# Kernel optimization log

Hardware: AMD Instinct MI355X
Metric: run time of the kernel (lower is better)

Reference implementation:

```python
import jax, jax.numpy as jnp
import numpy as np

B, L, H, NF = 8192, 2048, 2048, 8  # batch, latent, h_last_dim, n_flows


def setup_inputs() -> dict:
    key = jax.random.key(0)
    k0, k1, k2, k3 = jax.random.split(key, 4)
    scale = 0.02  # keep v well-conditioned through repeated linears
    return {
        "z": jax.random.normal(k0, (B, L), jnp.float32),
        "h_last": jax.random.normal(k1, (B, H), jnp.float32),
        "W0": jax.random.normal(k2, (L, H), jnp.float32) * scale,
        "b0": jnp.zeros((L,), jnp.float32),
        "Ws": jax.random.normal(k3, (NF - 1, L, L), jnp.float32) * scale,
        "bs": jnp.zeros((NF - 1, L), jnp.float32),
    }


def _hflow(v, z):
    # z_new = z - 2 * v (v . z) / ||v||^2  (Householder reflection, O(L) form of
    # the original's explicit vv^T bmm)
    vz = jnp.sum(v * z, axis=1, keepdims=True)       # [B,1]
    norm_sq = jnp.sum(v * v, axis=1, keepdims=True)  # [B,1]
    return z - 2.0 * v * (vz / norm_sq)


def reference(z, h_last, W0, b0, Ws, bs):
    # first v from h_last, then chain: v_{j+1} = Linear(v_j), z_{j+1} = HF(v_{j+1}, z_j)
    v = h_last @ W0.T + b0
    z = _hflow(v, z)

    def step(carry, wb):
        v, z = carry
        W, b = wb
        v = v @ W.T + b
        z = _hflow(v, z)
        return (v, z), None

    (v, z), _ = jax.lax.scan(step, (v, z), (Ws, bs))
    return z
```

## Files before the change

kernel.cpp:

```cpp
#include <hip/hip_runtime.h>
#include <hip/hip_bf16.h>
#include <stdint.h>

#define B_  8192
#define L_  2048
#define NF_ 8

typedef __bf16 bf16_t;
typedef __bf16 bf16x8 __attribute__((ext_vector_type(8)));
typedef __bf16 bf16x4 __attribute__((ext_vector_type(4)));
typedef float  floatx4 __attribute__((ext_vector_type(4)));

__device__ __forceinline__ bf16_t f2bf(float f) {
    union { float f; uint32_t u; } a; a.f = f;
    uint32_t r = a.u + 0x7fffu + ((a.u >> 16) & 1u);
    union { uint16_t s; bf16_t b; } o; o.s = (uint16_t)(r >> 16);
    return o.b;
}

#define GLD16(gp, lp)                                                          \
    __builtin_amdgcn_global_load_lds(                                          \
        (const __attribute__((address_space(1))) void*)(gp),                   \
        (__attribute__((address_space(3))) void*)(lp), 16, 0, 0)

__global__ __launch_bounds__(256) void cvt_kernel(const float* __restrict__ s,
                                                  bf16_t* __restrict__ d) {
    const int i = blockIdx.x * 256 + threadIdx.x;
    float4 f = ((const float4*)s)[i];
    bf16x4 o = { f2bf(f.x), f2bf(f.y), f2bf(f.z), f2bf(f.w) };
    ((bf16x4*)d)[i] = o;
}

__global__ __launch_bounds__(256, 4) void gemm_bt_kernel(
    const bf16_t* __restrict__ A,
    const bf16_t* __restrict__ W,
    const float*  __restrict__ bias,
    bf16_t* __restrict__ Vb)
{
    constexpr int K = L_;
    constexpr int N = L_;
    __shared__ alignas(16) bf16_t sA[128 * 64];
    __shared__ alignas(16) bf16_t sB[128 * 64];

    const int tid  = threadIdx.x;
    const int lane = tid & 63;
    const int wave = tid >> 6;
    const int wm   = wave >> 1;
    const int wn   = wave & 1;
    const int tm   = blockIdx.y * 128;
    const int tn   = blockIdx.x * 128;

    const int srow = tid >> 3;
    const int schk = (tid & 7) ^ (srow & 7);
    const bf16_t* Ag = A + (size_t)(tm + srow) * K + schk * 8;
    const bf16_t* Wg = W + (size_t)(tn + srow) * K + schk * 8;
    bf16_t* sAp = sA + tid * 8;
    bf16_t* sBp = sB + tid * 8;

    floatx4 acc[4][4] = {};

    const int ra = wm * 64 + (lane & 15);
    const int rb = wn * 64 + (lane & 15);
    const int q  = lane >> 4;
    const int rx = lane & 7;

    for (int kt = 0; kt < K; kt += 64) {
#pragma unroll
        for (int i = 0; i < 4; ++i) {
            GLD16(Ag + kt + (size_t)(32 * i) * K, sAp + i * 2048);
            GLD16(Wg + kt + (size_t)(32 * i) * K, sBp + i * 2048);
        }
        asm volatile("s_waitcnt vmcnt(0)" ::: "memory");
        __syncthreads();

#pragma unroll
        for (int ks = 0; ks < 2; ++ks) {
            const int c = ks * 4 + q;
            const int pc = (c ^ rx) * 8;
            bf16x8 af[4], bw[4];
#pragma unroll
            for (int i = 0; i < 4; ++i) {
                af[i] = *(const bf16x8*)(sA + (ra + i * 16) * 64 + pc);
                bw[i] = *(const bf16x8*)(sB + (rb + i * 16) * 64 + pc);
            }
#pragma unroll
            for (int mi = 0; mi < 4; ++mi)
#pragma unroll
                for (int ni = 0; ni < 4; ++ni)
                    acc[mi][ni] = __builtin_amdgcn_mfma_f32_16x16x32_bf16(
                        af[mi], bw[ni], acc[mi][ni], 0, 0, 0);
        }
        __syncthreads();
    }

    const int row0 = tm + wm * 64 + (lane >> 4) * 4;
    const int col0 = tn + wn * 64 + (lane & 15);
#pragma unroll
    for (int ni = 0; ni < 4; ++ni) {
        const int col = col0 + ni * 16;
        const float bv = bias[col];
#pragma unroll
        for (int mi = 0; mi < 4; ++mi) {
#pragma unroll
            for (int r = 0; r < 4; ++r) {
                Vb[(size_t)(row0 + mi * 16 + r) * N + col] = f2bf(acc[mi][ni][r] + bv);
            }
        }
    }
}

__global__ __launch_bounds__(256) void hflowN_kernel(
    const bf16_t* __restrict__ Vall,
    int nf,
    const float* __restrict__ zin, float* __restrict__ zout)
{
    const int lane = threadIdx.x & 63;
    const int row  = blockIdx.x * 4 + (threadIdx.x >> 6);
    const float4* z4 = (const float4*)(zin + (size_t)row * L_);
    float4*       zo = (float4*)(zout + (size_t)row * L_);

    float4 z[8];
#pragma unroll
    for (int j = 0; j < 4; ++j) {
        const int idx = lane + 64 * j;
        z[2 * j]     = z4[2 * idx];
        z[2 * j + 1] = z4[2 * idx + 1];
    }

    const size_t vstride = (size_t)B_ * L_;
    const bf16x8* v8 = (const bf16x8*)(Vall + (size_t)row * L_);

    bf16x8 vcur[4];
#pragma unroll
    for (int j = 0; j < 4; ++j) vcur[j] = v8[lane + 64 * j];

    for (int f = 0; f < nf; ++f) {
        bf16x8 vnxt[4];
        if (f + 1 < nf) {
            const bf16x8* vn = (const bf16x8*)((const bf16_t*)v8 + (size_t)(f + 1) * vstride);
#pragma unroll
            for (int j = 0; j < 4; ++j) vnxt[j] = vn[lane + 64 * j];
        }

        float vf[32];
#pragma unroll
        for (int j = 0; j < 4; ++j)
#pragma unroll
            for (int e = 0; e < 8; ++e) vf[j * 8 + e] = (float)vcur[j][e];

        float vz = 0.f, vv = 0.f;
#pragma unroll
        for (int j = 0; j < 4; ++j) {
            const float* fp = vf + j * 8;
            vz += fp[0] * z[2*j].x + fp[1] * z[2*j].y + fp[2] * z[2*j].z + fp[3] * z[2*j].w
                + fp[4] * z[2*j+1].x + fp[5] * z[2*j+1].y + fp[6] * z[2*j+1].z + fp[7] * z[2*j+1].w;
            vv += fp[0]*fp[0] + fp[1]*fp[1] + fp[2]*fp[2] + fp[3]*fp[3]
                + fp[4]*fp[4] + fp[5]*fp[5] + fp[6]*fp[6] + fp[7]*fp[7];
        }

#pragma unroll
        for (int off = 1; off < 64; off <<= 1) {
            vz += __shfl_xor(vz, off);
            vv += __shfl_xor(vv, off);
        }
        const float s = 2.0f * vz / vv;

#pragma unroll
        for (int j = 0; j < 4; ++j) {
            const float* fp = vf + j * 8;
            z[2*j].x -= s * fp[0]; z[2*j].y -= s * fp[1];
            z[2*j].z -= s * fp[2]; z[2*j].w -= s * fp[3];
            z[2*j+1].x -= s * fp[4]; z[2*j+1].y -= s * fp[5];
            z[2*j+1].z -= s * fp[6]; z[2*j+1].w -= s * fp[7];
        }

#pragma unroll
        for (int j = 0; j < 4; ++j) vcur[j] = vnxt[j];
    }

#pragma unroll
    for (int j = 0; j < 4; ++j) {
        const int idx = lane + 64 * j;
        zo[2 * idx]     = z[2 * j];
        zo[2 * idx + 1] = z[2 * j + 1];
    }
}

extern "C" void kernel_launch(void* const* d_in, const int* in_sizes, int n_in,
                              void* d_out, int out_size, void* d_ws, size_t ws_size,
                              hipStream_t stream) {
    (void)in_sizes; (void)n_in; (void)out_size;
    const float* z_in   = (const float*)d_in[0];
    const float* h_last = (const float*)d_in[1];
    const float* W0     = (const float*)d_in[2];
    const float* b0     = (const float*)d_in[3];
    const float* Wsp    = (const float*)d_in[4];
    const float* bsp    = (const float*)d_in[5];
    float* z_out = (float*)d_out;

    char* ws = (char*)d_ws;
    const size_t wbytes = (size_t)NF_ * L_ * L_ * 2;
    const size_t vbytes = (size_t)B_ * L_ * 2;

    bf16_t* Wbf = (bf16_t*)ws;
    cvt_kernel<<<(L_ * L_) / 1024, 256, 0, stream>>>(W0, Wbf);
    cvt_kernel<<<((NF_ - 1) * L_ * L_) / 1024, 256, 0, stream>>>(
        Wsp, Wbf + (size_t)L_ * L_);

    dim3 ggrid(L_ / 128, B_ / 128);

    if (ws_size >= wbytes + vbytes + (size_t)NF_ * vbytes) {
        bf16_t* Hbf  = (bf16_t*)(ws + wbytes);
        bf16_t* Vall = Hbf + (size_t)B_ * L_;
        cvt_kernel<<<(B_ * L_) / 1024, 256, 0, stream>>>(h_last, Hbf);

        for (int j = 0; j < NF_; ++j) {
            const float* bias = (j == 0) ? b0 : bsp + (size_t)(j - 1) * L_;
            const bf16_t* Wj = Wbf + (size_t)j * L_ * L_;
            const bf16_t* Ain = (j == 0) ? Hbf : Vall + (size_t)(j - 1) * B_ * L_;
            bf16_t* Vout = Vall + (size_t)j * B_ * L_;
            gemm_bt_kernel<<<ggrid, 256, 0, stream>>>(Ain, Wj, bias, Vout);
        }
        hflowN_kernel<<<B_ / 4, 256, 0, stream>>>(Vall, NF_, z_in, z_out);
    } else {
        bf16_t* Vp0 = (bf16_t*)(ws + wbytes);
        bf16_t* Vp1 = Vp0 + (size_t)B_ * L_;
        cvt_kernel<<<(B_ * L_) / 1024, 256, 0, stream>>>(h_last, Vp0);

        bf16_t* bufs[2] = { Vp0, Vp1 };
        for (int j = 0; j < NF_; ++j) {
            const float* bias = (j == 0) ? b0 : bsp + (size_t)(j - 1) * L_;
            const bf16_t* Wj = Wbf + (size_t)j * L_ * L_;
            bf16_t* Ain = bufs[j & 1];
            bf16_t* Vout = bufs[(j + 1) & 1];
            gemm_bt_kernel<<<ggrid, 256, 0, stream>>>(Ain, Wj, bias, Vout);
            hflowN_kernel<<<B_ / 4, 256, 0, stream>>>(
                Vout, 1, (j == 0) ? z_in : z_out, z_out);
        }
    }
}
```

Before: 889.1 us.

## Rewrite GEMM with 256x256 tiles, 4-stage LDS pipeline, and fused conversion kernel

```diff
diff --git a/kernel.cpp b/kernel.cpp
--- a/kernel.cpp
+++ b/kernel.cpp
@@ -23,87 +23,140 @@
         (const __attribute__((address_space(1))) void*)(gp),                   \
         (__attribute__((address_space(3))) void*)(lp), 16, 0, 0)
 
-__global__ __launch_bounds__(256) void cvt_kernel(const float* __restrict__ s,
-                                                  bf16_t* __restrict__ d) {
-    const int i = blockIdx.x * 256 + threadIdx.x;
-    float4 f = ((const float4*)s)[i];
-    bf16x4 o = { f2bf(f.x), f2bf(f.y), f2bf(f.z), f2bf(f.w) };
-    ((bf16x4*)d)[i] = o;
-}
-
-__global__ __launch_bounds__(256, 4) void gemm_bt_kernel(
+__global__ __launch_bounds__(256) void cvt3_kernel(
+    const float* __restrict__ sa, bf16_t* __restrict__ da, int na,
+    const float* __restrict__ sb, bf16_t* __restrict__ db, int nb,
+    const float* __restrict__ sc, bf16_t* __restrict__ dc, int nc)
+{
+    const int total = na + nb + nc;
+    for (int i = blockIdx.x * 256 + threadIdx.x; i < total;
+         i += gridDim.x * 256) {
+        const float* s; bf16_t* d; int j = i;
+        if (j < na)            { s = sa; d = da; }
+        else { j -= na;
+            if (j < nb)        { s = sb; d = db; }
+            else { j -= nb;      s = sc; d = dc; } }
+        float4 f = ((const float4*)s)[j];
+        bf16x4 o = { f2bf(f.x), f2bf(f.y), f2bf(f.z), f2bf(f.w) };
+        ((bf16x4*)d)[j] = o;
+    }
+}
+
+#define VM4  asm volatile("s_waitcnt vmcnt(4)" ::: "memory")
+#define VM0  asm volatile("s_waitcnt vmcnt(0)" ::: "memory")
+#define VMX  do {} while (0)
+
+__global__ __launch_bounds__(512, 2) void gemm_bt_kernel(
     const bf16_t* __restrict__ A,
     const bf16_t* __restrict__ W,
     const float*  __restrict__ bias,
     bf16_t* __restrict__ Vb)
 {
-    constexpr int K = L_;
-    constexpr int N = L_;
-    __shared__ alignas(16) bf16_t sA[128 * 64];
-    __shared__ alignas(16) bf16_t sB[128 * 64];
+    constexpr int K  = L_;
+    constexpr int N  = L_;
+    constexpr int NT = K / 32;
+    __shared__ alignas(16) bf16_t lds[4][16384];
 
     const int tid  = threadIdx.x;
     const int lane = tid & 63;
     const int wave = tid >> 6;
-    const int wm   = wave >> 1;
-    const int wn   = wave & 1;
-    const int tm   = blockIdx.y * 128;
-    const int tn   = blockIdx.x * 128;
-
-    const int srow = tid >> 3;
-    const int schk = (tid & 7) ^ (srow & 7);
-    const bf16_t* Ag = A + (size_t)(tm + srow) * K + schk * 8;
-    const bf16_t* Wg = W + (size_t)(tn + srow) * K + schk * 8;
-    bf16_t* sAp = sA + tid * 8;
-    bf16_t* sBp = sB + tid * 8;
-
-    floatx4 acc[4][4] = {};
-
-    const int ra = wm * 64 + (lane & 15);
-    const int rb = wn * 64 + (lane & 15);
-    const int q  = lane >> 4;
-    const int rx = lane & 7;
-
-    for (int kt = 0; kt < K; kt += 64) {
-#pragma unroll
-        for (int i = 0; i < 4; ++i) {
-            GLD16(Ag + kt + (size_t)(32 * i) * K, sAp + i * 2048);
-            GLD16(Wg + kt + (size_t)(32 * i) * K, sBp + i * 2048);
-        }
-        asm volatile("s_waitcnt vmcnt(0)" ::: "memory");
-        __syncthreads();
-
-#pragma unroll
-        for (int ks = 0; ks < 2; ++ks) {
-            const int c = ks * 4 + q;
-            const int pc = (c ^ rx) * 8;
-            bf16x8 af[4], bw[4];
-#pragma unroll
-            for (int i = 0; i < 4; ++i) {
-                af[i] = *(const bf16x8*)(sA + (ra + i * 16) * 64 + pc);
-                bw[i] = *(const bf16x8*)(sB + (rb + i * 16) * 64 + pc);
-            }
-#pragma unroll
-            for (int mi = 0; mi < 4; ++mi)
-#pragma unroll
-                for (int ni = 0; ni < 4; ++ni)
-                    acc[mi][ni] = __builtin_amdgcn_mfma_f32_16x16x32_bf16(
-                        af[mi], bw[ni], acc[mi][ni], 0, 0, 0);
-        }
-        __syncthreads();
-    }
-
-    const int row0 = tm + wm * 64 + (lane >> 4) * 4;
-    const int col0 = tn + wn * 64 + (lane & 15);
-#pragma unroll
-    for (int ni = 0; ni < 4; ++ni) {
-        const int col = col0 + ni * 16;
-        const float bv = bias[col];
-#pragma unroll
-        for (int mi = 0; mi < 4; ++mi) {
-#pragma unroll
-            for (int r = 0; r < 4; ++r) {
-                Vb[(size_t)(row0 + mi * 16 + r) * N + col] = f2bf(acc[mi][ni][r] + bv);
+    const int wm   = wave >> 2;
+    const int wn   = wave & 3;
+
+    const int wg  = blockIdx.x;
+    const int idx = wg >> 3;
+    const int bx  = idx >> 2;
+    const int by  = (wg & 7) * 4 + (idx & 3);
+    const int tm  = by * 256;
+    const int tn  = bx * 256;
+
+    const int r0 = tid >> 2;
+    const int lc = (tid & 3) ^ ((tid >> 3) & 3);
+    const bf16_t* Ag = A + (size_t)(tm + r0) * K + lc * 8;
+    const bf16_t* Wg = W + (size_t)(tn + r0) * K + lc * 8;
+    const int dA = tid * 8;
+    const int dB = 8192 + tid * 8;
+
+    const int l15  = lane & 15;
+    const int pc8  = (((lane >> 4) ^ ((l15 >> 1) & 3))) * 8;
+    const int aBase = (wm * 128 + l15) * 32 + pc8;
+    const int bBase = 8192 + (wn * 64 + l15) * 32 + pc8;
+
+    floatx4 acc[8][4] = {};
+
+    auto stageA = [&](int t) {
+        bf16_t* d = &lds[t & 3][dA];
+        const bf16_t* g = Ag + t * 32;
+        GLD16(g, d);
+        GLD16(g + (size_t)128 * K, d + 4096);
+    };
+    auto stageB = [&](int t) {
+        bf16_t* d = &lds[t & 3][dB];
+        const bf16_t* g = Wg + t * 32;
+        GLD16(g, d);
+        GLD16(g + (size_t)128 * K, d + 4096);
+    };
+
+    stageA(0); stageB(0);
+    stageA(1); stageB(1);
+    VM4;
+    asm volatile("s_barrier" ::: "memory");
+
+#define PHASE_MFMA(MB)                                                         \
+    __builtin_amdgcn_s_setprio(1);                                             \
+    _Pragma("unroll")                                                          \
+    for (int mi = 0; mi < 4; ++mi)                                             \
+        _Pragma("unroll")                                                      \
+        for (int ni = 0; ni < 4; ++ni)                                         \
+            acc[mi + (MB)][ni] = __builtin_amdgcn_mfma_f32_16x16x32_bf16(      \
+                af[mi], bw[ni], acc[mi + (MB)][ni], 0, 0, 0);                  \
+    __builtin_amdgcn_s_setprio(0);
+
+#define TILE_BODY(T, STG, VMCB)                                                \
+    {                                                                          \
+        const bf16_t* sl = &lds[(T) & 3][0];                                   \
+        bf16x8 af[4], bw[4];                                                   \
+           \
+        if (STG) stageA((T) + 2);                                              \
+        _Pragma("unroll")                                                      \
+        for (int ni = 0; ni < 4; ++ni)                                         \
+            bw[ni] = *(const bf16x8*)(sl + bBase + ni * 512);                  \
+        _Pragma("unroll")                                                      \
+        for (int mi = 0; mi < 4; ++mi)                                         \
+            af[mi] = *(const bf16x8*)(sl + aBase + mi * 512);                  \
+        asm volatile("s_barrier" ::: "memory");                                \
+        PHASE_MFMA(0)                                                          \
+        asm volatile("s_barrier" ::: "memory");                                \
+                \
+        if (STG) stageB((T) + 2);                                              \
+        _Pragma("unroll")                                                      \
+        for (int mi = 0; mi < 4; ++mi)                                         \
+            af[mi] = *(const bf16x8*)(sl + aBase + (mi + 4) * 512);            \
+        asm volatile("s_barrier" ::: "memory");                                \
+        PHASE_MFMA(4)                                                          \
+        VMCB;                                                                  \
+        asm volatile("s_barrier" ::: "memory");                                \
+    }
+
+    for (int t = 0; t < NT - 2; ++t) TILE_BODY(t, 1, VM4);
+    TILE_BODY(NT - 2, 0, VM0);
+    TILE_BODY(NT - 1, 0, VMX);
+#undef TILE_BODY
+#undef PHASE_MFMA
+
+    const int row0 = tm + wm * 128 + (lane >> 4) * 4;
+    const int col0 = tn + wn * 64 + l15;
+    float bv[4];
+#pragma unroll
+    for (int ni = 0; ni < 4; ++ni) bv[ni] = bias[col0 + ni * 16];
+#pragma unroll
+    for (int mi = 0; mi < 8; ++mi) {
+#pragma unroll
+        for (int r = 0; r < 4; ++r) {
+            const size_t ro = (size_t)(row0 + mi * 16 + r) * N;
+#pragma unroll
+            for (int ni = 0; ni < 4; ++ni) {
+                Vb[ro + col0 + ni * 16] = f2bf(acc[mi][ni][r] + bv[ni]);
             }
         }
     }
@@ -203,29 +256,33 @@
     const size_t vbytes = (size_t)B_ * L_ * 2;
 
     bf16_t* Wbf = (bf16_t*)ws;
-    cvt_kernel<<<(L_ * L_) / 1024, 256, 0, stream>>>(W0, Wbf);
-    cvt_kernel<<<((NF_ - 1) * L_ * L_) / 1024, 256, 0, stream>>>(
-        Wsp, Wbf + (size_t)L_ * L_);
-
-    dim3 ggrid(L_ / 128, B_ / 128);
+    const int grid = 256;
 
     if (ws_size >= wbytes + vbytes + (size_t)NF_ * vbytes) {
         bf16_t* Hbf  = (bf16_t*)(ws + wbytes);
         bf16_t* Vall = Hbf + (size_t)B_ * L_;
-        cvt_kernel<<<(B_ * L_) / 1024, 256, 0, stream>>>(h_last, Hbf);
+
+        cvt3_kernel<<<2048, 256, 0, stream>>>(
+            W0, Wbf, (L_ * L_) / 4,
+            Wsp, Wbf + (size_t)L_ * L_, ((NF_ - 1) * L_ * L_) / 4,
+            h_last, Hbf, (B_ * L_) / 4);
 
         for (int j = 0; j < NF_; ++j) {
             const float* bias = (j == 0) ? b0 : bsp + (size_t)(j - 1) * L_;
             const bf16_t* Wj = Wbf + (size_t)j * L_ * L_;
             const bf16_t* Ain = (j == 0) ? Hbf : Vall + (size_t)(j - 1) * B_ * L_;
             bf16_t* Vout = Vall + (size_t)j * B_ * L_;
-            gemm_bt_kernel<<<ggrid, 256, 0, stream>>>(Ain, Wj, bias, Vout);
+            gemm_bt_kernel<<<grid, 512, 0, stream>>>(Ain, Wj, bias, Vout);
         }
         hflowN_kernel<<<B_ / 4, 256, 0, stream>>>(Vall, NF_, z_in, z_out);
     } else {
         bf16_t* Vp0 = (bf16_t*)(ws + wbytes);
         bf16_t* Vp1 = Vp0 + (size_t)B_ * L_;
-        cvt_kernel<<<(B_ * L_) / 1024, 256, 0, stream>>>(h_last, Vp0);
+
+        cvt3_kernel<<<2048, 256, 0, stream>>>(
+            W0, Wbf, (L_ * L_) / 4,
+            Wsp, Wbf + (size_t)L_ * L_, ((NF_ - 1) * L_ * L_) / 4,
+            h_last, Vp0, (B_ * L_) / 4);
 
         bf16_t* bufs[2] = { Vp0, Vp1 };
         for (int j = 0; j < NF_; ++j) {
@@ -233,7 +290,7 @@
             const bf16_t* Wj = Wbf + (size_t)j * L_ * L_;
             bf16_t* Ain = bufs[j & 1];
             bf16_t* Vout = bufs[(j + 1) & 1];
-            gemm_bt_kernel<<<ggrid, 256, 0, stream>>>(Ain, Wj, bias, Vout);
+            gemm_bt_kernel<<<grid, 512, 0, stream>>>(Ain, Wj, bias, Vout);
             hflowN_kernel<<<B_ / 4, 256, 0, stream>>>(
                 Vout, 1, (j == 0) ? z_in : z_out, z_out);
         }
```

New measurement: 854.1 us. 1.04x faster.
